# Optimization experiments

Measured on AMD Instinct MI355X. Metric: run time of the kernel, lower is better.

Reference implementation:

```python
import jax, jax.numpy as jnp
import numpy as np
from jax import lax

TOP_NUMBER = 5
MOMENTUM = 0.1
EPS = 1e-12  # F.normalize eps


def _normalize(x):
    # F.normalize(x, dim=1): x / max(||x||_2, eps)
    n = jnp.sqrt(jnp.sum(x * x, axis=1, keepdims=True))
    return x / jnp.maximum(n, EPS)


def _cos_distance(a, b):
    # 0.5 * (1 - cos_sim); a:[B,D], b:[N,D] -> [B,N]
    a = _normalize(a)
    b = _normalize(b)
    return 0.5 * (1.0 - jnp.matmul(a, b.T))


def setup_inputs() -> dict:
    key = jax.random.key(0)
    ks = jax.random.split(key, 6)
    B, D, C, N = 64, 256, 345, 200000
    return {
        "target_feature": jax.random.normal(ks[0], (B, D), dtype=jnp.float32),
        "fc1": jax.random.normal(ks[1], (B, C), dtype=jnp.float32),
        "fc2": jax.random.normal(ks[2], (B, C), dtype=jnp.float32),
        "index_target": jnp.arange(B, dtype=jnp.int64 if jax.config.jax_enable_x64 else jnp.int32),
        "target_featurememory": jax.random.normal(ks[3], (N, D), dtype=jnp.float32),
        "target_softmaxFc1memory": jax.random.uniform(ks[4], (N, C), dtype=jnp.float32),
        "target_softmaxFc2memory": jax.random.uniform(ks[5], (N, C), dtype=jnp.float32),
    }


def reference(target_feature, fc1, fc2, index_target,
              target_featurememory, target_softmaxFc1memory, target_softmaxFc2memory):
    k = TOP_NUMBER
    m = MOMENTUM

    # predict(): softmax first
    fc1 = jax.nn.softmax(fc1, axis=1)
    fc2 = jax.nn.softmax(fc2, axis=1)

    # update(): momentum scatter-update of the memory banks (uses .data, i.e. detached)
    feat_mem = target_featurememory.at[index_target].set(
        (1.0 - m) * target_featurememory[index_target] + m * target_feature)
    fc1_mem = target_softmaxFc1memory.at[index_target].set(
        (1.0 - m) * target_softmaxFc1memory[index_target] + m * fc1)
    fc2_mem = target_softmaxFc2memory.at[index_target].set(
        (1.0 - m) * target_softmaxFc2memory[index_target] + m * fc2)

    # feature_smiliarity: nearest (smallest cos-distance) features, drop self (first)
    d_feat = _cos_distance(target_feature, feat_mem)          # [B, N]
    _, idx = lax.top_k(-d_feat, k + 1)                         # smallest distances
    idx = idx[:, 1:].reshape(-1)                               # [B*k]
    fc1_gather = fc1_mem[idx]                                  # [B*k, C]
    fc2_gather = fc2_mem[idx]
    loss_softmax = jnp.mean(jnp.abs(fc1_gather - fc2_gather))  # Discrepancy (L1)

    # softmax_smiliarity: topk of size k, then drop first -> k-1 neighbors
    d1 = _cos_distance(fc1, fc1_mem)                           # [B, N]
    _, i1 = lax.top_k(-d1, k)
    i1 = i1[:, 1:].reshape(-1)                                 # [B*(k-1)]
    feat1 = feat_mem[i1]                                       # [B*(k-1), D]

    d2 = _cos_distance(fc2, fc2_mem)
    _, i2 = lax.top_k(-d2, k)
    i2 = i2[:, 1:].reshape(-1)
    feat2 = feat_mem[i2]

    # FeatureDistance: 0.5 * (1 - <norm(a), norm(b)>) per row, then mean
    fd = 0.5 * (1.0 - jnp.sum(_normalize(feat1) * _normalize(feat2), axis=1))
    loss_feature = jnp.mean(fd)

    return (loss_softmax, loss_feature)
```

## Files before the change

kernel.cpp:

```cpp
#include <hip/hip_runtime.h>
#include <hip/hip_bf16.h>
#include <float.h>
#include <math.h>

#define NQ    64
#define DF    256
#define CC    345
#define KSF   8
#define KSC   11
#define NBM   768
#define FRESH (1 << 30)
#define EPSN  1e-12f

typedef __attribute__((ext_vector_type(8))) short short8;
typedef __attribute__((ext_vector_type(4))) float f32x4;

__device__ __forceinline__ void gld16(const void* g, void* l) {
  __builtin_amdgcn_global_load_lds(
      static_cast<const uint32_t*>(g), static_cast<uint32_t*>(l), 16, 0, 0);
}
__device__ __forceinline__ void gld4(const void* g, void* l) {
  __builtin_amdgcn_global_load_lds(
      static_cast<const uint32_t*>(g), static_cast<uint32_t*>(l), 4, 0, 0);
}

__device__ __forceinline__ void wait_vm0() {
  asm volatile("s_waitcnt vmcnt(0)" ::: "memory");
  __builtin_amdgcn_sched_barrier(0);
}
__device__ __forceinline__ void wait_vm4() {
  asm volatile("s_waitcnt vmcnt(4)" ::: "memory");
  __builtin_amdgcn_sched_barrier(0);
}
__device__ __forceinline__ void wait_vm8() {
  asm volatile("s_waitcnt vmcnt(8)" ::: "memory");
  __builtin_amdgcn_sched_barrier(0);
}
__device__ __forceinline__ void wait_vm9() {
  asm volatile("s_waitcnt vmcnt(9)" ::: "memory");
  __builtin_amdgcn_sched_barrier(0);
}
__device__ __forceinline__ void wait_lgkm0() {
  asm volatile("s_waitcnt lgkmcnt(0)" ::: "memory");
  __builtin_amdgcn_sched_barrier(0);
}
__device__ __forceinline__ void raw_barrier() {
  __builtin_amdgcn_sched_barrier(0);
  __builtin_amdgcn_s_barrier();
  __builtin_amdgcn_sched_barrier(0);
}

__global__ void zero_out(float* out) {
  if (threadIdx.x < 2) out[threadIdx.x] = 0.f;
}

__device__ __forceinline__ float blockReduceSum(float v, float* sbuf) {
  __syncthreads();
  #pragma unroll
  for (int o = 32; o > 0; o >>= 1) v += __shfl_down(v, o);
  int w = threadIdx.x >> 6;
  if ((threadIdx.x & 63) == 0) sbuf[w] = v;
  __syncthreads();
  if (threadIdx.x == 0) {
    float s = 0.f;
    int nw = blockDim.x >> 6;
    for (int i = 0; i < nw; ++i) s += sbuf[i];
    sbuf[0] = s;
  }
  __syncthreads();
  return sbuf[0];
}

__device__ __forceinline__ float blockReduceMax(float v, float* sbuf) {
  __syncthreads();
  #pragma unroll
  for (int o = 32; o > 0; o >>= 1) v = fmaxf(v, __shfl_down(v, o));
  int w = threadIdx.x >> 6;
  if ((threadIdx.x & 63) == 0) sbuf[w] = v;
  __syncthreads();
  if (threadIdx.x == 0) {
    float s = -FLT_MAX;
    int nw = blockDim.x >> 6;
    for (int i = 0; i < nw; ++i) s = fmaxf(s, sbuf[i]);
    sbuf[0] = s;
  }
  __syncthreads();
  return sbuf[0];
}

template<int T>
__device__ __forceinline__ void topk_insert(float v, int id, float (&lv)[T], int (&li)[T]) {
  if (!((v > lv[T-1]) || (v == lv[T-1] && id < li[T-1]))) return;
  #pragma unroll
  for (int p = T-1; p > 0; --p) {
    bool up = (v > lv[p-1]) || (v == lv[p-1] && id < li[p-1]);
    if (up) { lv[p] = lv[p-1]; li[p] = li[p-1]; }
    else    { lv[p] = v; li[p] = id; return; }
  }
  lv[0] = v; li[0] = id;
}

template<int T>
__device__ __forceinline__ void merge4(const float* sv, const int* si, int t,
                                       float* dv, int* di) {
  float fv[T]; int fi[T];
  #pragma unroll
  for (int i = 0; i < T; ++i) { fv[i] = -FLT_MAX; fi[i] = 0x7fffffff; }
  for (int s = 0; s < 4; ++s)
    #pragma unroll
    for (int i = 0; i < T; ++i)
      topk_insert<T>(sv[(t*4+s)*T+i], si[(t*4+s)*T+i], fv, fi);
  #pragma unroll
  for (int i = 0; i < T; ++i) { dv[t*T+i] = fv[i]; di[t*T+i] = fi[i]; }
}

__global__ void fill_rowmap(int* rowmap, int n) {
  int i = blockIdx.x * blockDim.x + threadIdx.x;
  if (i < n) rowmap[i] = -1;
}

__global__ __launch_bounds__(384) void prep_kernel(
    const float* __restrict__ tf, const float* __restrict__ fc1,
    const float* __restrict__ fc2, const int* __restrict__ idx,
    const float* __restrict__ featm, const float* __restrict__ fc1m,
    const float* __restrict__ fc2m,
    short* __restrict__ Qp_feat, short* __restrict__ Qp_fc1, short* __restrict__ Qp_fc2,
    float* __restrict__ featU, float* __restrict__ fc1U, float* __restrict__ fc2U,
    int* __restrict__ rowmap)
{
  __shared__ float sbuf[8];
  const int b = blockIdx.x, t = threadIdx.x;
  const int trow = idx[b];
  const int qt = b >> 4, qr = b & 15;

  {
    float x = (t < DF) ? tf[b*DF + t] : 0.f;
    float ss = blockReduceSum(x*x, sbuf);
    float inv = 1.f / fmaxf(sqrtf(ss), EPSN);
    if (t < DF) {
      featU[b*DF + t] = 0.9f * featm[(size_t)trow*DF + t] + 0.1f * x;
      int ks = t >> 5, lg = (t >> 3) & 3, j = t & 7;
      int lane = qr + lg*16;
      union { __hip_bfloat16 h; short s; } cv;
      cv.h = __float2bfloat16(x * inv);
      Qp_feat[((qt*KSF + ks)*64 + lane)*8 + j] = cv.s;
    }
  }
  {
    float y = (t < CC) ? fc1[b*CC + t] : -FLT_MAX;
    float mx = blockReduceMax(y, sbuf);
    float e = (t < CC) ? expf(y - mx) : 0.f;
    float se = blockReduceSum(e, sbuf);
    float s = e / se;
    float s2 = blockReduceSum(s*s, sbuf);
    float inv2 = 1.f / fmaxf(sqrtf(s2), EPSN);
    if (t < CC) fc1U[b*CC + t] = 0.9f * fc1m[(size_t)trow*CC + t] + 0.1f * s;
    if (t < KSC*32) {
      int ks = t >> 5, lg = (t >> 3) & 3, j = t & 7;
      int lane = qr + lg*16;
      union { __hip_bfloat16 h; short s; } cv;
      cv.h = __float2bfloat16((t < CC) ? s * inv2 : 0.f);
      Qp_fc1[((qt*KSC + ks)*64 + lane)*8 + j] = cv.s;
    }
  }
  {
    float y = (t < CC) ? fc2[b*CC + t] : -FLT_MAX;
    float mx = blockReduceMax(y, sbuf);
    float e = (t < CC) ? expf(y - mx) : 0.f;
    float se = blockReduceSum(e, sbuf);
    float s = e / se;
    float s2 = blockReduceSum(s*s, sbuf);
    float inv2 = 1.f / fmaxf(sqrtf(s2), EPSN);
    if (t < CC) fc2U[b*CC + t] = 0.9f * fc2m[(size_t)trow*CC + t] + 0.1f * s;
    if (t < KSC*32) {
      int ks = t >> 5, lg = (t >> 3) & 3, j = t & 7;
      int lane = qr + lg*16;
      union { __hip_bfloat16 h; short s; } cv;
      cv.h = __float2bfloat16((t < CC) ? s * inv2 : 0.f);
      Qp_fc2[((qt*KSC + ks)*64 + lane)*8 + j] = cv.s;
    }
  }
  if (t == 0) rowmap[trow] = b;
}

template<int D, int KS, int T>
__global__ __launch_bounds__(256, 3) void dist_topk6(
    const float* __restrict__ bank, const float* __restrict__ ubank,
    const int* __restrict__ uids, const short8* __restrict__ Qp,
    float* __restrict__ cand_v, int* __restrict__ cand_i,
    int nmain, int ntq, int ntr)
{
  constexpr bool FEAT = (D == 256);
  constexpr int GROW = D * 4;
  constexpr int SROW = FEAT ? 1024 : 1392;
  constexpr int BUFB = 16 * SROW;

  __shared__ __align__(16) char smem[2*BUFB + 128 + 2*64*17*4];
  char*  k344 = smem + 2*BUFB;
  float* sims = (float*)(smem + 2*BUFB + 128);
  float* mv   = (float*)smem;
  int*   mi   = (int*)(smem + 256*T*4);

  const int t = threadIdx.x, l = t & 63, w = t >> 6;
  const int lc = l & 15, lg = l >> 4;
  const bool corr = ((int)blockIdx.x >= nmain);
  const float* srcb = corr ? ubank : bank;

  int tile0, nt;
  if (corr) { tile0 = blockIdx.x - nmain; nt = 1; }
  else {
    int b = blockIdx.x;
    tile0 = b*ntq + (b < ntr ? b : ntr);
    nt = ntq + (b < ntr ? 1 : 0);
  }

  short8 afr[KS];
  #pragma unroll
  for (int ks = 0; ks < KS; ++ks) afr[ks] = Qp[(w*KS + ks)*64 + l];

  auto STAGE = [&](int tile, int pn) {
    const char* tb = (const char*)srcb + (size_t)tile * (size_t)(16*GROW);
    char* bb = smem + pn*BUFB;
    #pragma unroll
    for (int r2 = 0; r2 < 4; ++r2) {
      int row = w*4 + r2;
      if (FEAT) {
        gld16(tb + row*1024 + ((l ^ (row & 7)) * 16), bb + row*1024);
      } else {
        gld16(tb + row*1380 + l*16, bb + row*1392);
        if (l < 22) gld16(tb + row*1380 + 1024 + l*16, bb + row*1392 + 1024);
      }
    }
    if (!FEAT && w == 0 && l < 16)
      gld4(tb + l*1380 + 1376, k344 + pn*64);
  };

  STAGE(tile0, 0);
  if (nt > 1) STAGE(tile0 + 1, 1);

  float lv[T]; int li[T];
  #pragma unroll
  for (int i = 0; i < T; ++i) { lv[i] = -FLT_MAX; li[i] = 0x7fffffff; }

  for (int it = 0; it < nt; ++it) {
    const int pn = it & 1;

    if (it + 1 < nt) {
      if (FEAT) wait_vm4();
      else if (w == 0) wait_vm9();
      else wait_vm8();
    } else {
      wait_vm0();
    }
    raw_barrier();

    const char* bb = smem + pn*BUFB;
    f32x4 acc = (f32x4){0.f, 0.f, 0.f, 0.f};
    float sq = 0.f;

    #pragma unroll
    for (int ks = 0; ks < KS; ++ks) {
      float v[8];
      if (!FEAT && ks == KS-1 && lg == 3) {
        v[0] = *(const float*)(k344 + pn*64 + lc*4);
        #pragma unroll
        for (int j = 1; j < 8; ++j) v[j] = 0.f;
      } else if (FEAT) {
        int g0 = ks*8 + lg*2;
        float4 a = *(const float4*)(bb + lc*1024 + ((g0 ^ (lc & 7)) * 16));
        float4 c = *(const float4*)(bb + lc*1024 + (((g0 + 1) ^ (lc & 7)) * 16));
        v[0]=a.x; v[1]=a.y; v[2]=a.z; v[3]=a.w;
        v[4]=c.x; v[5]=c.y; v[6]=c.z; v[7]=c.w;
      } else {
        const char* p = bb + lc*1392 + ks*128 + lg*32;
        float4 a = *(const float4*)p;
        float4 c = *(const float4*)(p + 16);
        v[0]=a.x; v[1]=a.y; v[2]=a.z; v[3]=a.w;
        v[4]=c.x; v[5]=c.y; v[6]=c.z; v[7]=c.w;
      }
      #pragma unroll
      for (int j = 0; j < 8; ++j) sq += v[j]*v[j];
      union { short8 s8; __hip_bfloat162 h2[4]; } fb;
      #pragma unroll
      for (int j = 0; j < 4; ++j)
        fb.h2[j] = __float22bfloat162_rn(make_float2(v[2*j], v[2*j+1]));
      acc = __builtin_amdgcn_mfma_f32_16x16x32_bf16(afr[ks], fb.s8, acc, 0, 0, 0);
    }

    float s = sq;
    s += __shfl_xor(s, 16);
    s += __shfl_xor(s, 32);
    float ri = 1.f / fmaxf(sqrtf(s), EPSN);

    float* sp = sims + pn*64*17;
    #pragma unroll
    for (int rg = 0; rg < 4; ++rg)
      sp[(w*16 + lg*4 + rg)*17 + lc] = acc[rg] * ri;

    wait_lgkm0();
    raw_barrier();

    if (it + 2 < nt) STAGE(tile0 + it + 2, pn);

    {
      int q = t & 63, sub = t >> 6;
      const float* s2 = sims + pn*64*17 + q*17 + sub*4;
      #pragma unroll
      for (int j = 0; j < 4; ++j) {
        int r = sub*4 + j;
        int id = corr ? (uids[tile0*16 + r] | FRESH) : ((tile0 + it)*16 + r);
        topk_insert<T>(s2[j], id, lv, li);
      }
    }
  }
  __syncthreads();

  #pragma unroll
  for (int i = 0; i < T; ++i) { mv[t*T + i] = lv[i]; mi[t*T + i] = li[i]; }
  __syncthreads();
  if (t < 64) {
    float fv[T]; int fi[T];
    #pragma unroll
    for (int i = 0; i < T; ++i) { fv[i] = -FLT_MAX; fi[i] = 0x7fffffff; }
    for (int s = 0; s < 4; ++s) {
      int srcidx = t + 64*s;
      #pragma unroll
      for (int i = 0; i < T; ++i)
        topk_insert<T>(mv[srcidx*T + i], mi[srcidx*T + i], fv, fi);
    }
    size_t base = ((size_t)blockIdx.x*64 + t)*T;
    #pragma unroll
    for (int i = 0; i < T; ++i) { cand_v[base + i] = fv[i]; cand_i[base + i] = fi[i]; }
  }
}

template<int T>
__global__ __launch_bounds__(256) void merge_stage1(
    const float* __restrict__ cv, const int* __restrict__ ci,
    const int* __restrict__ rowmap, int nslots,
    float* __restrict__ midv, int* __restrict__ midi)
{
  __shared__ float sv[256*T]; __shared__ int si[256*T];
  __shared__ float sv2[64*T]; __shared__ int si2[64*T];
  const int q = blockIdx.x >> 3, s = blockIdx.x & 7, t = threadIdx.x;
  const int len = (nslots + 7) >> 3;
  const int lo = s*len, hi = min(nslots, lo + len);
  float lv[T]; int li[T];
  #pragma unroll
  for (int i = 0; i < T; ++i) { lv[i] = -FLT_MAX; li[i] = 0x7fffffff; }
  for (int c = lo + t; c < hi; c += 256) {
    size_t base = ((size_t)c*64 + q)*T;
    #pragma unroll
    for (int i = 0; i < T; ++i) {
      int id = ci[base + i];
      if ((id & FRESH) || rowmap[id] < 0)
        topk_insert<T>(cv[base + i], id, lv, li);
    }
  }
  #pragma unroll
  for (int i = 0; i < T; ++i) { sv[t*T+i] = lv[i]; si[t*T+i] = li[i]; }
  __syncthreads();
  if (t < 64) merge4<T>(sv, si, t, sv2, si2);
  __syncthreads();
  if (t < 16) merge4<T>(sv2, si2, t, sv, si);
  __syncthreads();
  if (t < 4)  merge4<T>(sv, si, t, sv2, si2);
  __syncthreads();
  if (t == 0) {
    float fv[T]; int fi[T];
    #pragma unroll
    for (int i = 0; i < T; ++i) { fv[i] = -FLT_MAX; fi[i] = 0x7fffffff; }
    for (int c = 0; c < 4*T; ++c) topk_insert<T>(sv2[c], si2[c], fv, fi);
    #pragma unroll
    for (int i = 0; i < T; ++i) {
      midv[blockIdx.x*T + i] = fv[i];
      midi[blockIdx.x*T + i] = fi[i];
    }
  }
}

template<int T>
__global__ __launch_bounds__(64) void merge_stage2(
    const float* __restrict__ midv, const int* __restrict__ midi,
    int* __restrict__ topout)
{
  __shared__ float sv[8*T]; __shared__ int si[8*T];
  const int q = blockIdx.x, t = threadIdx.x;
  if (t < 8*T) { sv[t] = midv[q*8*T + t]; si[t] = midi[q*8*T + t]; }
  __syncthreads();
  if (t == 0) {
    float fv[T]; int fi[T];
    #pragma unroll
    for (int i = 0; i < T; ++i) { fv[i] = -FLT_MAX; fi[i] = 0x7fffffff; }
    for (int c = 0; c < 8*T; ++c) topk_insert<T>(sv[c], si[c], fv, fi);
    #pragma unroll
    for (int i = 0; i < T; ++i) topout[q*6 + i] = fi[i] & ~FRESH;
  }
}

__global__ __launch_bounds__(384) void loss_softmax_kernel(
    const int* __restrict__ topfeat, const int* __restrict__ rowmap,
    const float* __restrict__ fc1m, const float* __restrict__ fc1U,
    const float* __restrict__ fc2m, const float* __restrict__ fc2U,
    float* __restrict__ out)
{
  __shared__ float sbuf[8];
  int p = blockIdx.x;
  int q = p / 5, j = p % 5 + 1;
  int row = topfeat[q*6 + j];
  int u = rowmap[row];
  const float* r1 = (u >= 0) ? (fc1U + (size_t)u * CC) : (fc1m + (size_t)row * CC);
  const float* r2 = (u >= 0) ? (fc2U + (size_t)u * CC) : (fc2m + (size_t)row * CC);
  int t = threadIdx.x;
  float v = (t < CC) ? fabsf(r1[t] - r2[t]) : 0.f;
  float s = blockReduceSum(v, sbuf);
  if (t == 0) atomicAdd(out, s * (1.f / (320.f * 345.f)));
}

__global__ __launch_bounds__(256) void loss_feature_kernel(
    const int* __restrict__ topfc1, const int* __restrict__ topfc2,
    const int* __restrict__ rowmap, const float* __restrict__ featm,
    const float* __restrict__ featU, float* __restrict__ out)
{
  __shared__ float sbuf[8];
  int p = blockIdx.x;
  int q = p / 4, j = p % 4 + 1;
  int ra = topfc1[q*6 + j], rb = topfc2[q*6 + j];
  int ua = rowmap[ra], ub = rowmap[rb];
  const float* A  = (ua >= 0) ? (featU + (size_t)ua * DF) : (featm + (size_t)ra * DF);
  const float* Bp = (ub >= 0) ? (featU + (size_t)ub * DF) : (featm + (size_t)rb * DF);
  int t = threadIdx.x;
  float a = A[t], b = Bp[t];
  float saa = blockReduceSum(a*a, sbuf);
  float sbb = blockReduceSum(b*b, sbuf);
  float sab = blockReduceSum(a*b, sbuf);
  if (t == 0) {
    float fd = 0.5f * (1.f - sab / (fmaxf(sqrtf(saa), EPSN) * fmaxf(sqrtf(sbb), EPSN)));
    atomicAdd(out + 1, fd * (1.f / 256.f));
  }
}

extern "C" void kernel_launch(void* const* d_in, const int* in_sizes, int n_in,
                              void* d_out, int out_size, void* d_ws, size_t ws_size,
                              hipStream_t stream)
{
  const float* tf    = (const float*)d_in[0];
  const float* fc1   = (const float*)d_in[1];
  const float* fc2   = (const float*)d_in[2];
  const int*   idx   = (const int*)d_in[3];
  const float* featm = (const float*)d_in[4];
  const float* fc1m  = (const float*)d_in[5];
  const float* fc2m  = (const float*)d_in[6];
  float* out = (float*)d_out;

  const int N     = in_sizes[4] / DF;
  const int TILES = N / 16;
  const int NTQ   = TILES / NBM;
  const int NTR   = TILES - NTQ * NBM;
  const int NSLOT = NBM + 4;

  char* w = (char*)d_ws;
  auto alloc = [&](size_t bytes) {
    char* p = w;
    w += (bytes + 255) & ~(size_t)255;
    return (void*)p;
  };
  short* Qp_feat = (short*)alloc((size_t)4 * KSF * 64 * 8 * 2);
  short* Qp_fc1  = (short*)alloc((size_t)4 * KSC * 64 * 8 * 2);
  short* Qp_fc2  = (short*)alloc((size_t)4 * KSC * 64 * 8 * 2);
  float* featU   = (float*)alloc((size_t)NQ * DF * 4);
  float* fc1U    = (float*)alloc((size_t)NQ * CC * 4);
  float* fc2U    = (float*)alloc((size_t)NQ * CC * 4);
  int*   rowmap  = (int*)alloc((size_t)N * 4);
  int*   topfeat = (int*)alloc(NQ * 6 * 4);
  int*   topfc1  = (int*)alloc(NQ * 6 * 4);
  int*   topfc2  = (int*)alloc(NQ * 6 * 4);
  float* cand_v  = (float*)alloc((size_t)NSLOT * 64 * 6 * 4);
  int*   cand_i  = (int*)alloc((size_t)NSLOT * 64 * 6 * 4);
  float* midv    = (float*)alloc((size_t)NQ * 8 * 6 * 4);
  int*   midi    = (int*)alloc((size_t)NQ * 8 * 6 * 4);

  zero_out<<<1, 64, 0, stream>>>(out);
  fill_rowmap<<<(N + 255) / 256, 256, 0, stream>>>(rowmap, N);
  prep_kernel<<<NQ, 384, 0, stream>>>(tf, fc1, fc2, idx, featm, fc1m, fc2m,
      Qp_feat, Qp_fc1, Qp_fc2, featU, fc1U, fc2U, rowmap);

  dist_topk6<DF, KSF, 6><<<NSLOT, 256, 0, stream>>>(
      featm, featU, idx, (const short8*)Qp_feat, cand_v, cand_i, NBM, NTQ, NTR);
  merge_stage1<6><<<NQ*8, 256, 0, stream>>>(cand_v, cand_i, rowmap, NSLOT, midv, midi);
  merge_stage2<6><<<NQ, 64, 0, stream>>>(midv, midi, topfeat);

  dist_topk6<CC, KSC, 5><<<NSLOT, 256, 0, stream>>>(
      fc1m, fc1U, idx, (const short8*)Qp_fc1, cand_v, cand_i, NBM, NTQ, NTR);
  merge_stage1<5><<<NQ*8, 256, 0, stream>>>(cand_v, cand_i, rowmap, NSLOT, midv, midi);
  merge_stage2<5><<<NQ, 64, 0, stream>>>(midv, midi, topfc1);

  dist_topk6<CC, KSC, 5><<<NSLOT, 256, 0, stream>>>(
      fc2m, fc2U, idx, (const short8*)Qp_fc2, cand_v, cand_i, NBM, NTQ, NTR);
  merge_stage1<5><<<NQ*8, 256, 0, stream>>>(cand_v, cand_i, rowmap, NSLOT, midv, midi);
  merge_stage2<5><<<NQ, 64, 0, stream>>>(midv, midi, topfc2);

  loss_softmax_kernel<<<320, 384, 0, stream>>>(topfeat, rowmap, fc1m, fc1U, fc2m, fc2U, out);
  loss_feature_kernel<<<256, 256, 0, stream>>>(topfc1, topfc2, rowmap, featm, featU, out);
}
```

Before: 678.1 us.

## Keep top-k per query in MFMA accumulator lanes, drop LDS sims staging and block merge

Swaps the MFMA operand order so each lane's accumulator holds four bank rows for a single query. Each lane then inserts its scores straight into its own register top-k, with row norms taken via shuffles. This removes the per-tile LDS store and reload of the similarity tile, and the end-of-block LDS reduction across the four waves. In exchange, every block writes four times as many candidate lists, which enlarges the merge_stage1 input. Each lane also performs all four inserts per tile itself, where before the work was spread across threads.

Measured after the change: 653.3 us. -3.6%, faster.

```diff
diff --git a/kernel.cpp b/kernel.cpp
--- a/kernel.cpp
+++ b/kernel.cpp
@@ -184,7 +184,7 @@
 }
 
 template<int D, int KS, int T>
-__global__ __launch_bounds__(256, 3) void dist_topk6(
+__global__ __launch_bounds__(256, 3) void dist_topk11(
     const float* __restrict__ bank, const float* __restrict__ ubank,
     const int* __restrict__ uids, const short8* __restrict__ Qp,
     float* __restrict__ cand_v, int* __restrict__ cand_i,
@@ -195,11 +195,8 @@
   constexpr int SROW = FEAT ? 1024 : 1392;
   constexpr int BUFB = 16 * SROW;
 
-  __shared__ __align__(16) char smem[2*BUFB + 128 + 2*64*17*4];
-  char*  k344 = smem + 2*BUFB;
-  float* sims = (float*)(smem + 2*BUFB + 128);
-  float* mv   = (float*)smem;
-  int*   mi   = (int*)(smem + 256*T*4);
+  __shared__ __align__(16) char smem[2*BUFB + 128];
+  char* k344 = smem + 2*BUFB;
 
   const int t = threadIdx.x, l = t & 63, w = t >> 6;
   const int lc = l & 15, lg = l >> 4;
@@ -284,54 +281,36 @@
       #pragma unroll
       for (int j = 0; j < 4; ++j)
         fb.h2[j] = __float22bfloat162_rn(make_float2(v[2*j], v[2*j+1]));
-      acc = __builtin_amdgcn_mfma_f32_16x16x32_bf16(afr[ks], fb.s8, acc, 0, 0, 0);
+      acc = __builtin_amdgcn_mfma_f32_16x16x32_bf16(fb.s8, afr[ks], acc, 0, 0, 0);
     }
 
     float s = sq;
     s += __shfl_xor(s, 16);
     s += __shfl_xor(s, 32);
-    float ri = 1.f / fmaxf(sqrtf(s), EPSN);
-
-    float* sp = sims + pn*64*17;
-    #pragma unroll
-    for (int rg = 0; rg < 4; ++rg)
-      sp[(w*16 + lg*4 + rg)*17 + lc] = acc[rg] * ri;
+    float ri_own = 1.f / fmaxf(sqrtf(s), EPSN);
+    float ri[4];
+    #pragma unroll
+    for (int j = 0; j < 4; ++j) ri[j] = __shfl(ri_own, lg*4 + j);
 
     wait_lgkm0();
     raw_barrier();
-
     if (it + 2 < nt) STAGE(tile0 + it + 2, pn);
 
-    {
-      int q = t & 63, sub = t >> 6;
-      const float* s2 = sims + pn*64*17 + q*17 + sub*4;
+    if (corr) {
       #pragma unroll
-      for (int j = 0; j < 4; ++j) {
-        int r = sub*4 + j;
-        int id = corr ? (uids[tile0*16 + r] | FRESH) : ((tile0 + it)*16 + r);
-        topk_insert<T>(s2[j], id, lv, li);
-      }
-    }
-  }
-  __syncthreads();
-
-  #pragma unroll
-  for (int i = 0; i < T; ++i) { mv[t*T + i] = lv[i]; mi[t*T + i] = li[i]; }
-  __syncthreads();
-  if (t < 64) {
-    float fv[T]; int fi[T];
-    #pragma unroll
-    for (int i = 0; i < T; ++i) { fv[i] = -FLT_MAX; fi[i] = 0x7fffffff; }
-    for (int s = 0; s < 4; ++s) {
-      int srcidx = t + 64*s;
+      for (int j = 0; j < 4; ++j)
+        topk_insert<T>(acc[j] * ri[j], uids[tile0*16 + lg*4 + j] | FRESH, lv, li);
+    } else {
+      const int gb = (tile0 + it) * 16 + lg*4;
       #pragma unroll
-      for (int i = 0; i < T; ++i)
-        topk_insert<T>(mv[srcidx*T + i], mi[srcidx*T + i], fv, fi);
-    }
-    size_t base = ((size_t)blockIdx.x*64 + t)*T;
-    #pragma unroll
-    for (int i = 0; i < T; ++i) { cand_v[base + i] = fv[i]; cand_i[base + i] = fi[i]; }
-  }
+      for (int j = 0; j < 4; ++j)
+        topk_insert<T>(acc[j] * ri[j], gb + j, lv, li);
+    }
+  }
+
+  size_t base = (((size_t)blockIdx.x*4 + lg)*64 + w*16 + lc)*T;
+  #pragma unroll
+  for (int i = 0; i < T; ++i) { cand_v[base + i] = lv[i]; cand_i[base + i] = li[i]; }
 }
 
 template<int T>
@@ -457,7 +436,8 @@
   const int TILES = N / 16;
   const int NTQ   = TILES / NBM;
   const int NTR   = TILES - NTQ * NBM;
-  const int NSLOT = NBM + 4;
+  const int NBLKS = NBM + 4;
+  const int NSLOT = NBLKS * 4;
 
   char* w = (char*)d_ws;
   auto alloc = [&](size_t bytes) {
@@ -485,17 +465,17 @@
   prep_kernel<<<NQ, 384, 0, stream>>>(tf, fc1, fc2, idx, featm, fc1m, fc2m,
       Qp_feat, Qp_fc1, Qp_fc2, featU, fc1U, fc2U, rowmap);
 
-  dist_topk6<DF, KSF, 6><<<NSLOT, 256, 0, stream>>>(
+  dist_topk11<DF, KSF, 6><<<NBLKS, 256, 0, stream>>>(
       featm, featU, idx, (const short8*)Qp_feat, cand_v, cand_i, NBM, NTQ, NTR);
   merge_stage1<6><<<NQ*8, 256, 0, stream>>>(cand_v, cand_i, rowmap, NSLOT, midv, midi);
   merge_stage2<6><<<NQ, 64, 0, stream>>>(midv, midi, topfeat);
 
-  dist_topk6<CC, KSC, 5><<<NSLOT, 256, 0, stream>>>(
+  dist_topk11<CC, KSC, 5><<<NBLKS, 256, 0, stream>>>(
       fc1m, fc1U, idx, (const short8*)Qp_fc1, cand_v, cand_i, NBM, NTQ, NTR);
   merge_stage1<5><<<NQ*8, 256, 0, stream>>>(cand_v, cand_i, rowmap, NSLOT, midv, midi);
   merge_stage2<5><<<NQ, 64, 0, stream>>>(midv, midi, topfc1);
 
-  dist_topk6<CC, KSC, 5><<<NSLOT, 256, 0, stream>>>(
+  dist_topk11<CC, KSC, 5><<<NBLKS, 256, 0, stream>>>(
       fc2m, fc2U, idx, (const short8*)Qp_fc2, cand_v, cand_i, NBM, NTQ, NTR);
   merge_stage1<5><<<NQ*8, 256, 0, stream>>>(cand_v, cand_i, rowmap, NSLOT, midv, midi);
   merge_stage2<5><<<NQ, 64, 0, stream>>>(midv, midi, topfc2);
```
